# Kernel tuning notes

Measured on AMD Instinct MI355X. Metric: run time of the kernel, lower is better.

The kernel has to match this reference:

```python
import jax, jax.numpy as jnp
import numpy as np

N, E, DIN, H, DOUT = 100000, 400000, 128, 128, 128
LN_EPS = 1e-5


def _layernorm(x, g, b):
    m = jnp.mean(x, axis=-1, keepdims=True)
    v = jnp.mean((x - m) ** 2, axis=-1, keepdims=True)
    return (x - m) * jax.lax.rsqrt(v + LN_EPS) * g + b


def setup_inputs() -> dict:
    key = jax.random.key(0)
    ks = jax.random.split(key, 24)
    s = 1.0 / np.sqrt(H)
    inp = {
        'feat': jax.random.normal(ks[0], (N, DIN), jnp.float32),
        'edge_src': jax.random.randint(ks[1], (E,), 0, N, jnp.int32),
        'edge_dst': jax.random.randint(ks[2], (E,), 0, N, jnp.int32),
        'W_src': jax.random.normal(ks[3], (DIN, H), jnp.float32) * s,
        'b_src': jax.random.normal(ks[4], (H,), jnp.float32) * s,
        'W_dst': jax.random.normal(ks[5], (DIN, H), jnp.float32) * s,
        'b_dst': jax.random.normal(ks[6], (H,), jnp.float32) * s,
        'W1a': jax.random.normal(ks[7], (H, H), jnp.float32) * s,
        'W1b': jax.random.normal(ks[8], (H, H), jnp.float32) * s,
        'b1': jax.random.normal(ks[9], (H,), jnp.float32) * s,
        'W2': jax.random.normal(ks[10], (H, H), jnp.float32) * s,
        'b2': jax.random.normal(ks[11], (H,), jnp.float32) * s,
        'W3': jax.random.normal(ks[12], (H, H), jnp.float32) * s,
        'b3': jax.random.normal(ks[13], (H,), jnp.float32) * s,
        'ln_g': jnp.ones((H,), jnp.float32),
        'ln_b': jnp.zeros((H,), jnp.float32),
        'Wg1a': jax.random.normal(ks[14], (H, H), jnp.float32) * s,
        'Wg1b': jax.random.normal(ks[15], (H, H), jnp.float32) * s,
        'bg1': jax.random.normal(ks[16], (H,), jnp.float32) * s,
        'Wg2': jax.random.normal(ks[17], (H, 1), jnp.float32) * s,
        'bg2': jax.random.normal(ks[18], (1,), jnp.float32) * s,
        'W_out': jax.random.normal(ks[19], (H, DOUT), jnp.float32) * s,
        'b_out': jax.random.normal(ks[20], (DOUT,), jnp.float32) * s,
    }
    return inp


def reference(feat, edge_src, edge_dst, W_src, b_src, W_dst, b_dst,
              W1a, W1b, b1, W2, b2, W3, b3, ln_g, ln_b,
              Wg1a, Wg1b, bg1, Wg2, bg2, W_out, b_out):
    gelu = lambda x: jax.nn.gelu(x, approximate=False)  # torch nn.GELU default (erf)
    # node-level src/dst transforms, then gather per edge
    src_h = feat @ W_src + b_src                 # [N,H]
    dst_h = feat @ W_dst + b_dst                 # [N,H]
    se = src_h[edge_src]                         # [E,H]
    de = dst_h[edge_dst]                         # [E,H]
    # edge MLP on concat([se,de]) expressed as split weights (same math)
    h = gelu(se @ W1a + de @ W1b + b1)           # [E,H]
    h = gelu(h @ W2 + b2)                        # [E,H]
    msg = _layernorm(h @ W3 + b3, ln_g, ln_b)    # [E,H]
    # message gating
    gate = jax.nn.sigmoid(gelu(se @ Wg1a + de @ Wg1b + bg1) @ Wg2 + bg2)  # [E,1]
    msg = gate * msg
    # scatter-sum to destination nodes, then out transform
    upd = jax.ops.segment_sum(msg, edge_dst, num_segments=N)  # [N,H]
    return upd @ W_out + b_out                   # [N,DOUT]
```

## Files before the change

### kernel.cpp

```cpp
#include <hip/hip_runtime.h>
#include <hip/hip_bf16.h>
#include <math.h>


typedef __bf16 bf16x8 __attribute__((ext_vector_type(8)));
typedef float floatx4 __attribute__((ext_vector_type(4)));

#define LN_EPS 1e-5f

__device__ __forceinline__ unsigned short f2bf(float x) {
  unsigned int u = __float_as_uint(x);
  u = u + 0x7fffu + ((u >> 16) & 1u);
  return (unsigned short)(u >> 16);
}

__device__ __forceinline__ float bf2f(unsigned short s) {
  return __uint_as_float(((unsigned int)s) << 16);
}

__device__ __forceinline__ float geluf(float x) {
  float t = x * x;
  float u = x * (2.3022080f + 0.1029434f * t);
  float e = __builtin_amdgcn_exp2f(-u);
  return x * __builtin_amdgcn_rcpf(1.0f + e);
}

__device__ __forceinline__ float sigmoidf_fast(float x) {
  float e = __builtin_amdgcn_exp2f(-1.44269504f * x);
  return __builtin_amdgcn_rcpf(1.0f + e);
}

__global__ __launch_bounds__(256) void prep_weights(
    const float* w0, const float* w1, const float* w2, const float* w3,
    const float* w4, const float* w5, const float* w6, const float* w7,
    const float* w8, unsigned short* out) {
  const float* srcs[9] = {w0, w1, w2, w3, w4, w5, w6, w7, w8};
  int m = blockIdx.x >> 2, c = blockIdx.x & 3;
  const float* src = srcs[m] + c * 32 * 128;
  __shared__ unsigned short sT[128][35];
  int tid = threadIdx.x;

  for (int it = 0; it < 4; ++it) {
    int f4 = tid + it * 256;
    float4 v = ((const float4*)src)[f4];
    int krel = f4 >> 5;
    int n0 = (f4 & 31) * 4;
    sT[n0 + 0][krel] = f2bf(v.x);
    sT[n0 + 1][krel] = f2bf(v.y);
    sT[n0 + 2][krel] = f2bf(v.z);
    sT[n0 + 3][krel] = f2bf(v.w);
  }
  __syncthreads();
  unsigned short* dst = out + m * 16384 + c * 32;
  for (int it = 0; it < 2; ++it) {
    int ch = tid + it * 256;
    int n = ch >> 2, kc = (ch & 3) * 8;
    unsigned short tmp[8];
    for (int j = 0; j < 8; ++j) tmp[j] = sT[n][kc + j];
    *(int4*)(dst + n * 128 + kc) = *(const int4*)tmp;
  }
}

#define LDB(pB, B)                                              \
  do {                                                          \
    const unsigned short* _p = (pB);                            \
    for (int kb = 0; kb < 4; ++kb) {                            \
      B[0][kb] = *(const bf16x8*)(_p + kb * 32);                \
      B[1][kb] = *(const bf16x8*)(_p + 2048 + kb * 32);         \
    }                                                           \
  } while (0)

__global__ __launch_bounds__(256, 4) void node_fused(
    const float* __restrict__ feat, const unsigned short* __restrict__ wT,
    const float* __restrict__ b_src, const float* __restrict__ b_dst,
    const float* __restrict__ b1, const float* __restrict__ bg1,
    unsigned short* __restrict__ SrcCat, unsigned short* __restrict__ DstCat,
    unsigned short* __restrict__ upd, int M) {
  __shared__ __align__(16) unsigned short sF[64][136];
  __shared__ __align__(16) unsigned short sT[64][136];
  int tid = threadIdx.x;
  int r0 = blockIdx.x * 64;
  int y = blockIdx.y;

  if (y == 0) {
    int4 z = {0, 0, 0, 0};
    int4* p = (int4*)(upd + (long long)r0 * 128);
    for (int it = 0; it < 4; ++it) {
      int idx = tid + it * 256;
      if (r0 + (idx >> 4) < M) p[idx] = z;
    }
  }

  {
    int r = tid >> 2, seg = tid & 3;
    int row = r0 + r;
    const float* src = feat + (long long)row * 128;
    for (int it = 0; it < 4; ++it) {
      int c = (seg * 4 + it) * 8;
      unsigned short tmp[8];
      if (row < M) {
        float4 f0 = *(const float4*)(src + c);
        float4 f1 = *(const float4*)(src + c + 4);
        tmp[0] = f2bf(f0.x); tmp[1] = f2bf(f0.y); tmp[2] = f2bf(f0.z); tmp[3] = f2bf(f0.w);
        tmp[4] = f2bf(f1.x); tmp[5] = f2bf(f1.y); tmp[6] = f2bf(f1.z); tmp[7] = f2bf(f1.w);
      } else {
        for (int j = 0; j < 8; ++j) tmp[j] = 0;
      }
      *(int4*)&sF[r][c] = *(const int4*)tmp;
    }
  }
  __syncthreads();

  int w = tid >> 6, lane = tid & 63, lr = lane & 15, q = lane >> 4;
  int c0 = 32 * w + lr, c1 = 32 * w + 16 + lr;
  const unsigned short* pB = wT + c0 * 128 + q * 8;

  const unsigned short* wH = pB + (y ? 1 : 0) * 16384;
  const unsigned short* wA = pB + (y ? 3 : 2) * 16384;
  const unsigned short* wG = pB + (y ? 7 : 6) * 16384;
  unsigned short* Cat = y ? DstCat : SrcCat;
  float hb0 = y ? b_dst[c0] : b_src[c0];
  float hb1 = y ? b_dst[c1] : b_src[c1];
  float ab0 = y ? 0.f : b1[c0];
  float ab1 = y ? 0.f : b1[c1];
  float gb0 = y ? 0.f : bg1[c0];
  float gb1 = y ? 0.f : bg1[c1];

  bf16x8 B[2][4];

  auto pass = [&](const unsigned short (*Ab)[136], floatx4 (&acc)[4][2]) {
    for (int kb = 0; kb < 4; ++kb) {
      int k = kb * 32 + q * 8;
      for (int mb = 0; mb < 4; ++mb) {
        bf16x8 a = *(const bf16x8*)&Ab[16 * mb + lr][k];
        acc[mb][0] = __builtin_amdgcn_mfma_f32_16x16x32_bf16(a, B[0][kb], acc[mb][0], 0, 0, 0);
        acc[mb][1] = __builtin_amdgcn_mfma_f32_16x16x32_bf16(a, B[1][kb], acc[mb][1], 0, 0, 0);
      }
    }
  };

  {
    floatx4 acc[4][2];
    for (int mb = 0; mb < 4; ++mb)
      for (int nb = 0; nb < 2; ++nb) acc[mb][nb] = (floatx4){0.f, 0.f, 0.f, 0.f};
    LDB(wH, B);
    pass(sF, acc);
    for (int mb = 0; mb < 4; ++mb)
      for (int i = 0; i < 4; ++i) {
        int r = 16 * mb + 4 * q + i;
        sT[r][c0] = f2bf(acc[mb][0][i] + hb0);
        sT[r][c1] = f2bf(acc[mb][1][i] + hb1);
      }
  }
  __syncthreads();

  floatx4 accA[4][2], accP[4][2];
  for (int mb = 0; mb < 4; ++mb)
    for (int nb = 0; nb < 2; ++nb) {
      accA[mb][nb] = (floatx4){0.f, 0.f, 0.f, 0.f};
      accP[mb][nb] = (floatx4){0.f, 0.f, 0.f, 0.f};
    }
  LDB(wA, B);
  pass(sT, accA);
  LDB(wG, B);
  pass(sT, accP);
  __syncthreads();

  for (int mb = 0; mb < 4; ++mb)
    for (int i = 0; i < 4; ++i) {
      int r = 16 * mb + 4 * q + i;
      sF[r][c0] = f2bf(accA[mb][0][i] + ab0);
      sF[r][c1] = f2bf(accA[mb][1][i] + ab1);
      sT[r][c0] = f2bf(accP[mb][0][i] + gb0);
      sT[r][c1] = f2bf(accP[mb][1][i] + gb1);
    }
  __syncthreads();

  for (int it = 0; it < 8; ++it) {
    int idx = tid + it * 256;
    int row = idx >> 5, c = idx & 31;
    if (r0 + row < M) {
      const void* src = (c < 16) ? (const void*)&sF[row][c * 8]
                                 : (const void*)&sT[row][(c - 16) * 8];
      *(int4*)(Cat + (long long)(r0 + row) * 256 + c * 8) = *(const int4*)src;
    }
  }
}

__global__ __launch_bounds__(256, 4) void gemm_out(
    const unsigned short* __restrict__ A, const unsigned short* __restrict__ Bt,
    const float* __restrict__ bias, float* __restrict__ C, int M) {
  __shared__ __align__(16) char smem[64 * 130 * 4];
  unsigned short (*sA)[136] = (unsigned short(*)[136])smem;
  float (*sO)[130] = (float(*)[130])smem;
  int tid = threadIdx.x;
  int r0 = blockIdx.x * 64;

  {
    int r = tid >> 2, seg = tid & 3;
    int row = r0 + r;
    const int4* src = (const int4*)(A + (long long)row * 128);
    for (int it = 0; it < 4; ++it) {
      int c = seg * 4 + it;
      int4 v;
      if (row < M) v = src[c];
      else v = (int4){0, 0, 0, 0};
      *(int4*)&sA[r][c * 8] = v;
    }
  }
  __syncthreads();

  int w = tid >> 6, lane = tid & 63, lr = lane & 15, q = lane >> 4;
  int c0 = 32 * w + lr, c1 = 32 * w + 16 + lr;
  const unsigned short* pB = Bt + c0 * 128 + q * 8;

  bf16x8 B[2][4];
  LDB(pB, B);
  floatx4 acc[4][2];
  for (int mb = 0; mb < 4; ++mb)
    for (int nb = 0; nb < 2; ++nb) acc[mb][nb] = (floatx4){0.f, 0.f, 0.f, 0.f};
  for (int kb = 0; kb < 4; ++kb) {
    int k = kb * 32 + q * 8;
    for (int mb = 0; mb < 4; ++mb) {
      bf16x8 a = *(const bf16x8*)&sA[16 * mb + lr][k];
      acc[mb][0] = __builtin_amdgcn_mfma_f32_16x16x32_bf16(a, B[0][kb], acc[mb][0], 0, 0, 0);
      acc[mb][1] = __builtin_amdgcn_mfma_f32_16x16x32_bf16(a, B[1][kb], acc[mb][1], 0, 0, 0);
    }
  }
  __syncthreads();

  float bv0 = bias[c0], bv1 = bias[c1];
  for (int mb = 0; mb < 4; ++mb)
    for (int i = 0; i < 4; ++i) {
      int r = 16 * mb + 4 * q + i;
      sO[r][c0] = acc[mb][0][i] + bv0;
      sO[r][c1] = acc[mb][1][i] + bv1;
    }
  __syncthreads();

  for (int it = 0; it < 8; ++it) {
    int idx = tid + it * 256;
    int row = idx >> 5, c = idx & 31;
    if (r0 + row < M)
      *(float4*)(C + (long long)(r0 + row) * 128 + c * 4) = *(const float4*)&sO[row][c * 4];
  }
}

__global__ __launch_bounds__(256, 6) void edge_fused(
    const unsigned short* __restrict__ SrcCat, const unsigned short* __restrict__ DstCat,
    const int* __restrict__ edge_src, const int* __restrict__ edge_dst,
    const unsigned short* __restrict__ wT,
    const float* __restrict__ b2, const float* __restrict__ b3,
    const float* __restrict__ ln_g, const float* __restrict__ ln_b,
    const float* __restrict__ Wg2, const float* __restrict__ bg2,
    unsigned short* __restrict__ upd, int E) {
  __shared__ __align__(16) unsigned short sH[64][136];
  __shared__ int sDst[64];
  __shared__ float sGate[64];
  __shared__ float sR1[4][64];
  __shared__ float sR2[4][64];
  __shared__ float sM[64];
  __shared__ float sRS[64];

  int tid = threadIdx.x;
  int e0 = blockIdx.x * 64;

  {
    int r = tid >> 2, seg = tid & 3;
    int e = e0 + r;
    int ee = (e < E) ? e : (E - 1);
    int es = edge_src[ee], ed = edge_dst[ee];
    if (seg == 0) sDst[r] = (e < E) ? ed : -1;
    const unsigned short* ps = SrcCat + (long long)es * 256 + seg * 32;
    const unsigned short* pd = DstCat + (long long)ed * 256 + seg * 32;

    int4 sa[4], sb[4], ga[4], gb[4];
    for (int u = 0; u < 4; ++u) {
      sa[u] = ((const int4*)ps)[u];
      sb[u] = ((const int4*)pd)[u];
      ga[u] = ((const int4*)(ps + 128))[u];
      gb[u] = ((const int4*)(pd + 128))[u];
    }
    for (int u = 0; u < 4; ++u) {
      const unsigned short* av = (const unsigned short*)&sa[u];
      const unsigned short* bv = (const unsigned short*)&sb[u];
      unsigned short outv[8];
      for (int j = 0; j < 8; ++j)
        outv[j] = f2bf(geluf(bf2f(av[j]) + bf2f(bv[j])));
      *(int4*)&sH[r][seg * 32 + u * 8] = *(const int4*)outv;
    }
    float gp = 0.f;
    for (int u = 0; u < 4; ++u) {
      const unsigned short* av = (const unsigned short*)&ga[u];
      const unsigned short* bv = (const unsigned short*)&gb[u];
      float4 w0 = *(const float4*)(Wg2 + seg * 32 + u * 8);
      float4 w1 = *(const float4*)(Wg2 + seg * 32 + u * 8 + 4);
      gp += geluf(bf2f(av[0]) + bf2f(bv[0])) * w0.x;
      gp += geluf(bf2f(av[1]) + bf2f(bv[1])) * w0.y;
      gp += geluf(bf2f(av[2]) + bf2f(bv[2])) * w0.z;
      gp += geluf(bf2f(av[3]) + bf2f(bv[3])) * w0.w;
      gp += geluf(bf2f(av[4]) + bf2f(bv[4])) * w1.x;
      gp += geluf(bf2f(av[5]) + bf2f(bv[5])) * w1.y;
      gp += geluf(bf2f(av[6]) + bf2f(bv[6])) * w1.z;
      gp += geluf(bf2f(av[7]) + bf2f(bv[7])) * w1.w;
    }
    gp += __shfl_xor(gp, 1);
    gp += __shfl_xor(gp, 2);
    if (seg == 0) sGate[r] = sigmoidf_fast(gp + bg2[0]);
  }
  __syncthreads();

  int w = tid >> 6, lane = tid & 63, lr = lane & 15, q = lane >> 4;
  int c0 = 32 * w + lr, c1 = 32 * w + 16 + lr;
  const unsigned short* pB = wT + c0 * 128 + q * 8;

  bf16x8 B[2][4];
  floatx4 acc[4][2];
  auto zacc = [&]() {
    for (int mb = 0; mb < 4; ++mb)
      for (int nb = 0; nb < 2; ++nb) acc[mb][nb] = (floatx4){0.f, 0.f, 0.f, 0.f};
  };
  auto pass = [&](const unsigned short (*Ab)[136]) {
    for (int kb = 0; kb < 4; ++kb) {
      int k = kb * 32 + q * 8;
      for (int mb = 0; mb < 4; ++mb) {
        bf16x8 a = *(const bf16x8*)&Ab[16 * mb + lr][k];
        acc[mb][0] = __builtin_amdgcn_mfma_f32_16x16x32_bf16(a, B[0][kb], acc[mb][0], 0, 0, 0);
        acc[mb][1] = __builtin_amdgcn_mfma_f32_16x16x32_bf16(a, B[1][kb], acc[mb][1], 0, 0, 0);
      }
    }
  };

  LDB(pB + 4 * 16384, B);
  zacc();
  pass(sH);
  __syncthreads();
  {
    float bv0 = b2[c0], bv1 = b2[c1];
    for (int mb = 0; mb < 4; ++mb)
      for (int i = 0; i < 4; ++i) {
        int r = 16 * mb + 4 * q + i;
        sH[r][c0] = f2bf(geluf(acc[mb][0][i] + bv0));
        sH[r][c1] = f2bf(geluf(acc[mb][1][i] + bv1));
      }
  }
  __syncthreads();

  LDB(pB + 5 * 16384, B);
  zacc();
  pass(sH);
  {
    float bv0 = b3[c0], bv1 = b3[c1];
    for (int mb = 0; mb < 4; ++mb)
      for (int i = 0; i < 4; ++i) {
        float x0 = acc[mb][0][i] + bv0;
        float x1 = acc[mb][1][i] + bv1;
        acc[mb][0][i] = x0; acc[mb][1][i] = x1;
        float s = x0 + x1, s2 = x0 * x0 + x1 * x1;
        s += __shfl_xor(s, 1); s += __shfl_xor(s, 2);
        s += __shfl_xor(s, 4); s += __shfl_xor(s, 8);
        s2 += __shfl_xor(s2, 1); s2 += __shfl_xor(s2, 2);
        s2 += __shfl_xor(s2, 4); s2 += __shfl_xor(s2, 8);
        if (lr == 0) { sR1[w][16 * mb + 4 * q + i] = s; sR2[w][16 * mb + 4 * q + i] = s2; }
      }
  }
  __syncthreads();
  if (tid < 64) {
    float s = sR1[0][tid] + sR1[1][tid] + sR1[2][tid] + sR1[3][tid];
    float s2 = sR2[0][tid] + sR2[1][tid] + sR2[2][tid] + sR2[3][tid];
    float m = s * (1.f / 128.f);
    float v = s2 * (1.f / 128.f) - m * m;
    sM[tid] = m;
    sRS[tid] = rsqrtf(v + LN_EPS);
  }
  __syncthreads();

  {
    float lg0 = ln_g[c0], lg1 = ln_g[c1];
    float lb0 = ln_b[c0], lb1 = ln_b[c1];
    for (int mb = 0; mb < 4; ++mb)
      for (int i = 0; i < 4; ++i) {
        int r = 16 * mb + 4 * q + i;
        int dst = sDst[r];
        float m = sM[r], rs = sRS[r], gt = sGate[r];
        float v0 = ((acc[mb][0][i] - m) * rs * lg0 + lb0) * gt;
        float v1 = ((acc[mb][1][i] - m) * rs * lg1 + lb1) * gt;
        float o0 = __shfl_xor(v0, 1);
        float o1 = __shfl_xor(v1, 1);
        if (dst >= 0) {
          unsigned int pk;
          int colb;
          if ((lr & 1) == 0) {
            pk = (unsigned int)f2bf(v0) | ((unsigned int)f2bf(o0) << 16);
            colb = c0;
          } else {
            pk = (unsigned int)f2bf(o1) | ((unsigned int)f2bf(v1) << 16);
            colb = c0 + 15;
          }
          unsigned short* addr = upd + (long long)dst * 128 + colb;
          asm volatile("global_atomic_pk_add_bf16 %0, %1, off"
                       :: "v"(addr), "v"(pk) : "memory");
        }
      }
  }
}

extern "C" void kernel_launch(void* const* d_in, const int* in_sizes, int n_in,
                              void* d_out, int out_size, void* d_ws, size_t ws_size,
                              hipStream_t stream) {
  const float* feat   = (const float*)d_in[0];
  const int* edge_src = (const int*)d_in[1];
  const int* edge_dst = (const int*)d_in[2];
  const float* W_src = (const float*)d_in[3];  const float* b_src = (const float*)d_in[4];
  const float* W_dst = (const float*)d_in[5];  const float* b_dst = (const float*)d_in[6];
  const float* W1a = (const float*)d_in[7];    const float* W1b = (const float*)d_in[8];
  const float* b1  = (const float*)d_in[9];
  const float* W2  = (const float*)d_in[10];   const float* b2  = (const float*)d_in[11];
  const float* W3  = (const float*)d_in[12];   const float* b3  = (const float*)d_in[13];
  const float* ln_g = (const float*)d_in[14];  const float* ln_b = (const float*)d_in[15];
  const float* Wg1a = (const float*)d_in[16];  const float* Wg1b = (const float*)d_in[17];
  const float* bg1  = (const float*)d_in[18];
  const float* Wg2  = (const float*)d_in[19];  const float* bg2 = (const float*)d_in[20];
  const float* W_out = (const float*)d_in[21]; const float* b_out = (const float*)d_in[22];

  int N = in_sizes[0] / 128;
  int E = in_sizes[1];

  char* ws = (char*)d_ws;
  unsigned short* wT = (unsigned short*)ws;
  size_t off = 9 * 16384 * sizeof(unsigned short);
  unsigned short* SrcCat = (unsigned short*)(ws + off);
  off += (size_t)N * 256 * sizeof(unsigned short);
  unsigned short* DstCat = (unsigned short*)(ws + off);
  off += (size_t)N * 256 * sizeof(unsigned short);
  unsigned short* upd = (unsigned short*)(ws + off);

  prep_weights<<<36, 256, 0, stream>>>(W_src, W_dst, W1a, W1b, W2, W3, Wg1a, Wg1b,
                                       W_out, wT);
  int mtiles = (N + 63) / 64;
  node_fused<<<dim3(mtiles, 2), 256, 0, stream>>>(feat, wT, b_src, b_dst, b1, bg1,
                                                  SrcCat, DstCat, upd, N);
  edge_fused<<<(E + 63) / 64, 256, 0, stream>>>(SrcCat, DstCat, edge_src, edge_dst,
                                                wT, b2, b3, ln_g, ln_b, Wg2, bg2,
                                                upd, E);
  gemm_out<<<mtiles, 256, 0, stream>>>(upd, wT + 8 * 16384, b_out, (float*)d_out, N);
}
```

Measured before the change: 369.3 us.

## Merge src/dst node passes per block, pack bf16 conversions, split edge launch

Result: slower. 429.6 us (+16.3%).

```diff
diff --git a/kernel.cpp b/kernel.cpp
--- a/kernel.cpp
+++ b/kernel.cpp
@@ -4,6 +4,7 @@
 
 
 typedef __bf16 bf16x8 __attribute__((ext_vector_type(8)));
+typedef __bf16 bf16x2 __attribute__((ext_vector_type(2)));
 typedef float floatx4 __attribute__((ext_vector_type(4)));
 
 #define LN_EPS 1e-5f
@@ -12,6 +13,13 @@
   unsigned int u = __float_as_uint(x);
   u = u + 0x7fffu + ((u >> 16) & 1u);
   return (unsigned short)(u >> 16);
+}
+
+__device__ __forceinline__ unsigned int pkbf(float lo, float hi) {
+  bf16x2 v;
+  v.x = (__bf16)lo;
+  v.y = (__bf16)hi;
+  return __builtin_bit_cast(unsigned int, v);
 }
 
 __device__ __forceinline__ float bf2f(unsigned short s) {
@@ -80,9 +88,8 @@
   __shared__ __align__(16) unsigned short sT[64][136];
   int tid = threadIdx.x;
   int r0 = blockIdx.x * 64;
-  int y = blockIdx.y;
-
-  if (y == 0) {
+
+  {
     int4 z = {0, 0, 0, 0};
     int4* p = (int4*)(upd + (long long)r0 * 128);
     for (int it = 0; it < 4; ++it) {
@@ -94,40 +101,38 @@
   {
     int r = tid >> 2, seg = tid & 3;
     int row = r0 + r;
-    const float* src = feat + (long long)row * 128;
-    for (int it = 0; it < 4; ++it) {
-      int c = (seg * 4 + it) * 8;
-      unsigned short tmp[8];
+    const float* src = feat + (long long)row * 128 + seg * 32;
+    for (int j = 0; j < 4; ++j) {
+      unsigned int tmp[4];
       if (row < M) {
-        float4 f0 = *(const float4*)(src + c);
-        float4 f1 = *(const float4*)(src + c + 4);
-        tmp[0] = f2bf(f0.x); tmp[1] = f2bf(f0.y); tmp[2] = f2bf(f0.z); tmp[3] = f2bf(f0.w);
-        tmp[4] = f2bf(f1.x); tmp[5] = f2bf(f1.y); tmp[6] = f2bf(f1.z); tmp[7] = f2bf(f1.w);
+        float4 f0 = *(const float4*)(src + j * 8);
+        float4 f1 = *(const float4*)(src + j * 8 + 4);
+        tmp[0] = pkbf(f0.x, f0.y);
+        tmp[1] = pkbf(f0.z, f0.w);
+        tmp[2] = pkbf(f1.x, f1.y);
+        tmp[3] = pkbf(f1.z, f1.w);
       } else {
-        for (int j = 0; j < 8; ++j) tmp[j] = 0;
-      }
-      *(int4*)&sF[r][c] = *(const int4*)tmp;
+        tmp[0] = tmp[1] = tmp[2] = tmp[3] = 0;
+      }
+      *(int4*)&sF[r][seg * 32 + j * 8] = *(const int4*)tmp;
     }
   }
   __syncthreads();
 
   int w = tid >> 6, lane = tid & 63, lr = lane & 15, q = lane >> 4;
-  int c0 = 32 * w + lr, c1 = 32 * w + 16 + lr;
+  int c0 = 32 * w + lr, c1 = c0 + 16;
   const unsigned short* pB = wT + c0 * 128 + q * 8;
 
-  const unsigned short* wH = pB + (y ? 1 : 0) * 16384;
-  const unsigned short* wA = pB + (y ? 3 : 2) * 16384;
-  const unsigned short* wG = pB + (y ? 7 : 6) * 16384;
-  unsigned short* Cat = y ? DstCat : SrcCat;
-  float hb0 = y ? b_dst[c0] : b_src[c0];
-  float hb1 = y ? b_dst[c1] : b_src[c1];
-  float ab0 = y ? 0.f : b1[c0];
-  float ab1 = y ? 0.f : b1[c1];
-  float gb0 = y ? 0.f : bg1[c0];
-  float gb1 = y ? 0.f : bg1[c1];
-
   bf16x8 B[2][4];
-
+  floatx4 accA[4][2], accP[4][2];
+
+  auto zacc2 = [&]() {
+    for (int mb = 0; mb < 4; ++mb)
+      for (int nb = 0; nb < 2; ++nb) {
+        accA[mb][nb] = (floatx4){0.f, 0.f, 0.f, 0.f};
+        accP[mb][nb] = (floatx4){0.f, 0.f, 0.f, 0.f};
+      }
+  };
   auto pass = [&](const unsigned short (*Ab)[136], floatx4 (&acc)[4][2]) {
     for (int kb = 0; kb < 4; ++kb) {
       int k = kb * 32 + q * 8;
@@ -138,53 +143,58 @@
       }
     }
   };
-
-  {
-    floatx4 acc[4][2];
-    for (int mb = 0; mb < 4; ++mb)
-      for (int nb = 0; nb < 2; ++nb) acc[mb][nb] = (floatx4){0.f, 0.f, 0.f, 0.f};
-    LDB(wH, B);
-    pass(sF, acc);
+  auto store_cat = [&](unsigned short* base, floatx4 (&acc)[4][2],
+                       float bb0, float bb1) {
+    for (int mb = 0; mb < 4; ++mb)
+      for (int i = 0; i < 4; ++i) {
+        int rr = 16 * mb + 4 * q + i;
+        int row = r0 + rr;
+        float v0 = acc[mb][0][i] + bb0;
+        float v1 = acc[mb][1][i] + bb1;
+        float o0 = __shfl_xor(v0, 1);
+        float o1 = __shfl_xor(v1, 1);
+        unsigned int pk;
+        int colb;
+        if ((lr & 1) == 0) { pk = pkbf(v0, o0); colb = c0; }
+        else               { pk = pkbf(o1, v1); colb = c0 + 15; }
+        if (row < M)
+          *(unsigned int*)(base + (long long)row * 256 + colb) = pk;
+      }
+  };
+  auto h_pass = [&](const unsigned short* wh, float hb0, float hb1) {
+    for (int mb = 0; mb < 4; ++mb)
+      for (int nb = 0; nb < 2; ++nb) accA[mb][nb] = (floatx4){0.f, 0.f, 0.f, 0.f};
+    LDB(wh, B);
+    pass(sF, accA);
     for (int mb = 0; mb < 4; ++mb)
       for (int i = 0; i < 4; ++i) {
         int r = 16 * mb + 4 * q + i;
-        sT[r][c0] = f2bf(acc[mb][0][i] + hb0);
-        sT[r][c1] = f2bf(acc[mb][1][i] + hb1);
-      }
-  }
-  __syncthreads();
-
-  floatx4 accA[4][2], accP[4][2];
-  for (int mb = 0; mb < 4; ++mb)
-    for (int nb = 0; nb < 2; ++nb) {
-      accA[mb][nb] = (floatx4){0.f, 0.f, 0.f, 0.f};
-      accP[mb][nb] = (floatx4){0.f, 0.f, 0.f, 0.f};
-    }
-  LDB(wA, B);
+        unsigned int u = pkbf(accA[mb][0][i] + hb0, accA[mb][1][i] + hb1);
+        sT[r][c0] = (unsigned short)u;
+        sT[r][c1] = (unsigned short)(u >> 16);
+      }
+  };
+
+  h_pass(pB + 0 * 16384, b_src[c0], b_src[c1]);
+  __syncthreads();
+  zacc2();
+  LDB(pB + 2 * 16384, B);
   pass(sT, accA);
-  LDB(wG, B);
+  LDB(pB + 6 * 16384, B);
   pass(sT, accP);
-  __syncthreads();
-
-  for (int mb = 0; mb < 4; ++mb)
-    for (int i = 0; i < 4; ++i) {
-      int r = 16 * mb + 4 * q + i;
-      sF[r][c0] = f2bf(accA[mb][0][i] + ab0);
-      sF[r][c1] = f2bf(accA[mb][1][i] + ab1);
-      sT[r][c0] = f2bf(accP[mb][0][i] + gb0);
-      sT[r][c1] = f2bf(accP[mb][1][i] + gb1);
-    }
-  __syncthreads();
-
-  for (int it = 0; it < 8; ++it) {
-    int idx = tid + it * 256;
-    int row = idx >> 5, c = idx & 31;
-    if (r0 + row < M) {
-      const void* src = (c < 16) ? (const void*)&sF[row][c * 8]
-                                 : (const void*)&sT[row][(c - 16) * 8];
-      *(int4*)(Cat + (long long)(r0 + row) * 256 + c * 8) = *(const int4*)src;
-    }
-  }
+  store_cat(SrcCat,       accA, b1[c0],  b1[c1]);
+  store_cat(SrcCat + 128, accP, bg1[c0], bg1[c1]);
+  __syncthreads();
+
+  h_pass(pB + 1 * 16384, b_dst[c0], b_dst[c1]);
+  __syncthreads();
+  zacc2();
+  LDB(pB + 3 * 16384, B);
+  pass(sT, accA);
+  LDB(pB + 7 * 16384, B);
+  pass(sT, accP);
+  store_cat(DstCat,       accA, 0.f, 0.f);
+  store_cat(DstCat + 128, accP, 0.f, 0.f);
 }
 
 __global__ __launch_bounds__(256, 4) void gemm_out(
@@ -284,10 +294,13 @@
     for (int u = 0; u < 4; ++u) {
       const unsigned short* av = (const unsigned short*)&sa[u];
       const unsigned short* bv = (const unsigned short*)&sb[u];
-      unsigned short outv[8];
-      for (int j = 0; j < 8; ++j)
-        outv[j] = f2bf(geluf(bf2f(av[j]) + bf2f(bv[j])));
-      *(int4*)&sH[r][seg * 32 + u * 8] = *(const int4*)outv;
+      unsigned int ov[4];
+      for (int j = 0; j < 4; ++j) {
+        float g0 = geluf(bf2f(av[2 * j])     + bf2f(bv[2 * j]));
+        float g1 = geluf(bf2f(av[2 * j + 1]) + bf2f(bv[2 * j + 1]));
+        ov[j] = pkbf(g0, g1);
+      }
+      *(int4*)&sH[r][seg * 32 + u * 8] = *(const int4*)ov;
     }
     float gp = 0.f;
     for (int u = 0; u < 4; ++u) {
@@ -340,8 +353,9 @@
     for (int mb = 0; mb < 4; ++mb)
       for (int i = 0; i < 4; ++i) {
         int r = 16 * mb + 4 * q + i;
-        sH[r][c0] = f2bf(geluf(acc[mb][0][i] + bv0));
-        sH[r][c1] = f2bf(geluf(acc[mb][1][i] + bv1));
+        unsigned int u = pkbf(geluf(acc[mb][0][i] + bv0), geluf(acc[mb][1][i] + bv1));
+        sH[r][c0] = (unsigned short)u;
+        sH[r][c1] = (unsigned short)(u >> 16);
       }
   }
   __syncthreads();
@@ -391,10 +405,10 @@
           unsigned int pk;
           int colb;
           if ((lr & 1) == 0) {
-            pk = (unsigned int)f2bf(v0) | ((unsigned int)f2bf(o0) << 16);
+            pk = pkbf(v0, o0);
             colb = c0;
           } else {
-            pk = (unsigned int)f2bf(o1) | ((unsigned int)f2bf(v1) << 16);
+            pk = pkbf(o1, v1);
             colb = c0 + 15;
           }
           unsigned short* addr = upd + (long long)dst * 128 + colb;
@@ -438,10 +452,15 @@
   prep_weights<<<36, 256, 0, stream>>>(W_src, W_dst, W1a, W1b, W2, W3, Wg1a, Wg1b,
                                        W_out, wT);
   int mtiles = (N + 63) / 64;
-  node_fused<<<dim3(mtiles, 2), 256, 0, stream>>>(feat, wT, b_src, b_dst, b1, bg1,
-                                                  SrcCat, DstCat, upd, N);
-  edge_fused<<<(E + 63) / 64, 256, 0, stream>>>(SrcCat, DstCat, edge_src, edge_dst,
-                                                wT, b2, b3, ln_g, ln_b, Wg2, bg2,
-                                                upd, E);
+  node_fused<<<mtiles, 256, 0, stream>>>(feat, wT, b_src, b_dst, b1, bg1,
+                                         SrcCat, DstCat, upd, N);
+  int Eh = E / 2;
+  edge_fused<<<(Eh + 63) / 64, 256, 0, stream>>>(SrcCat, DstCat, edge_src, edge_dst,
+                                                 wT, b2, b3, ln_g, ln_b, Wg2, bg2,
+                                                 upd, Eh);
+  edge_fused<<<((E - Eh) + 63) / 64, 256, 0, stream>>>(SrcCat, DstCat,
+                                                 edge_src + Eh, edge_dst + Eh,
+                                                 wT, b2, b3, ln_g, ln_b, Wg2, bg2,
+                                                 upd, E - Eh);
   gemm_out<<<mtiles, 256, 0, stream>>>(upd, wT + 8 * 16384, b_out, (float*)d_out, N);
 }
```
